# Kernel tuning notes

Measured on AMD Instinct MI355X. Metric: run time of the kernel, lower is better.

The kernel has to match this reference:

```python
import jax, jax.numpy as jnp
import numpy as np

INPUT_DIM = 512
OUTPUT_DIM = 32
DEGREE = 8


def setup_inputs() -> dict:
    key = jax.random.key(0)
    kx, kw = jax.random.split(key)
    x = jax.random.normal(kx, (65536, INPUT_DIM), dtype=jnp.float32)
    # xavier_normal_ on [input_dim, output_dim, degree+1]: torch treats last dims as fan;
    # fan_in = output_dim*(degree+1), fan_out = input_dim*(degree+1)
    fan_in = OUTPUT_DIM * (DEGREE + 1)
    fan_out = INPUT_DIM * (DEGREE + 1)
    std = float(np.sqrt(2.0 / (fan_in + fan_out)))
    cheby_coeffs = std * jax.random.normal(kw, (INPUT_DIM, OUTPUT_DIM, DEGREE + 1), dtype=jnp.float32)
    return {"x": x, "cheby_coeffs": cheby_coeffs}


def reference(x, cheby_coeffs):
    xt = jnp.tanh(x.reshape(-1, INPUT_DIM))
    T = [jnp.ones_like(xt), 2.0 * xt]
    for n in range(2, DEGREE + 1):
        T.append(2.0 * xt * T[n - 1] - T[n - 2])
    T = jnp.stack(T, axis=-1)  # [B, I, degree+1]
    y = jnp.einsum('bij,ioj->bo', T, cheby_coeffs)  # [B, O]
    return y
```

## Files before the change

### kernel.cpp

```cpp
#include <hip/hip_runtime.h>
#include <hip/hip_fp16.h>


typedef _Float16 half8 __attribute__((ext_vector_type(8)));
typedef __fp16  fp16x2 __attribute__((ext_vector_type(2)));
typedef float float4v __attribute__((ext_vector_type(4)));

#define N_I 512
#define N_O 32
#define N_PERIODS 8
#define STEPS 8
#define CHUNK_F16 8192
#define PERIOD_F16 16384
#define PERIOD_BYTES 32768

__global__ void prep(const float* __restrict__ coeffs, _Float16* __restrict__ bsw,
                     float* __restrict__ bias) {
    if (blockIdx.x == 512) {
        int o = threadIdx.x >> 3, p = threadIdx.x & 7;
        float s = 0.f;
        for (int i = p; i < N_I; i += 8) s += coeffs[(i * 32 + o) * 9];
        for (int off = 4; off; off >>= 1) s += __shfl_down(s, off, 8);
        if (p == 0) bias[o] = s;
        return;
    }
    int id = blockIdx.x * 256 + threadIdx.x;
    int jj = id & 7;
    int L  = (id >> 3) & 63;
    int t  = (id >> 9) & 1;
    int s  = id >> 10;
    int ci = s >> 3, sl = s & 7;
    int j  = sl + 1;
    int ii = ((L >> 4) << 3) + jj;
    int i  = ci * 32 + ii;
    int o  = t * 16 + (L & 15);
    bsw[id] = (_Float16)coeffs[(i * 32 + o) * 9 + j];
}

__device__ __forceinline__ float fast_tanh(float v) {
    float e = __expf(2.0f * v);
    return __builtin_fmaf(-2.0f, __builtin_amdgcn_rcpf(e + 1.0f), 1.0f);
}

__device__ __forceinline__ half8 pack8(const float* u) {
    union { fp16x2 h[4]; half8 v; } r;
    r.h[0] = __builtin_amdgcn_cvt_pkrtz(u[0], u[1]);
    r.h[1] = __builtin_amdgcn_cvt_pkrtz(u[2], u[3]);
    r.h[2] = __builtin_amdgcn_cvt_pkrtz(u[4], u[5]);
    r.h[3] = __builtin_amdgcn_cvt_pkrtz(u[6], u[7]);
    return r.v;
}

__global__ __launch_bounds__(256, 2) void cheby_main(
        const float* __restrict__ x, const _Float16* __restrict__ bsw,
        const float* __restrict__ bias, float* __restrict__ y) {
    __shared__ __align__(16) _Float16 bl[2][PERIOD_F16];

    const int tid = threadIdx.x;
    const int wv  = tid >> 6;
    const int L   = tid & 63;
    const int q   = L >> 4;
    const int mr  = L & 15;
    const int m0  = blockIdx.x * 128 + wv * 32;
    const float* xr0 = x + (size_t)(m0 + mr) * N_I + q * 8;
    const float* xr1 = xr0 + 16 * N_I;
    const char* gB = (const char*)bsw;

    float4v acc[2][2];
#pragma unroll
    for (int a = 0; a < 2; ++a)
#pragma unroll
        for (int b = 0; b < 2; ++b)
#pragma unroll
            for (int e = 0; e < 4; ++e) acc[a][b][e] = 0.f;

    auto stage = [&](int p, int buf) {
        const char* gsrc = gB + (size_t)p * PERIOD_BYTES + wv * 8192 + L * 16;
        char* lds = (char*)&bl[buf][0] + wv * 8192;
#pragma unroll
        for (int it = 0; it < 8; ++it) {
            __builtin_amdgcn_global_load_lds(
                (const __attribute__((address_space(1))) void*)(gsrc + it * 1024),
                (__attribute__((address_space(3))) void*)(lds + it * 1024),
                16, 0, 0);
        }
    };

    auto loadx = [&](int p, float4v* v) {
#pragma unroll
        for (int c = 0; c < 2; ++c) {
            const int o = (p * 2 + c) * 32;
            v[c * 4 + 0] = *(const float4v*)(xr0 + o);
            v[c * 4 + 1] = *(const float4v*)(xr0 + o + 4);
            v[c * 4 + 2] = *(const float4v*)(xr1 + o);
            v[c * 4 + 3] = *(const float4v*)(xr1 + o + 4);
        }
    };

    auto chunk = [&](const _Float16* bb, float4v xa, float4v xb,
                     float4v xc, float4v xd) {
        float w0[8], w1[8], up0[8], uc0[8], up1[8], uc1[8];
#pragma unroll
        for (int e = 0; e < 4; ++e) {
            w0[e]     = 2.0f * fast_tanh(xa[e]);
            w0[e + 4] = 2.0f * fast_tanh(xb[e]);
            w1[e]     = 2.0f * fast_tanh(xc[e]);
            w1[e + 4] = 2.0f * fast_tanh(xd[e]);
        }
#pragma unroll
        for (int e = 0; e < 8; ++e) {
            up0[e] = 1.0f; uc0[e] = w0[e];
            up1[e] = 1.0f; uc1[e] = w1[e];
        }
#pragma unroll
        for (int s = 0; s < STEPS; ++s) {
            const half8 a0 = pack8(uc0);
            const half8 a1 = pack8(uc1);
            const half8 b0 = *(const half8*)(bb + (s * 2 + 0) * 512 + L * 8);
            const half8 b1 = *(const half8*)(bb + (s * 2 + 1) * 512 + L * 8);
            acc[0][0] = __builtin_amdgcn_mfma_f32_16x16x32_f16(a0, b0, acc[0][0], 0, 0, 0);
            acc[0][1] = __builtin_amdgcn_mfma_f32_16x16x32_f16(a0, b1, acc[0][1], 0, 0, 0);
            acc[1][0] = __builtin_amdgcn_mfma_f32_16x16x32_f16(a1, b0, acc[1][0], 0, 0, 0);
            acc[1][1] = __builtin_amdgcn_mfma_f32_16x16x32_f16(a1, b1, acc[1][1], 0, 0, 0);
#pragma unroll
            for (int e = 0; e < 8; ++e) {
                float n0 = __builtin_fmaf(w0[e], uc0[e], -up0[e]);
                float n1 = __builtin_fmaf(w1[e], uc1[e], -up1[e]);
                up0[e] = uc0[e]; uc0[e] = n0;
                up1[e] = uc1[e]; uc1[e] = n1;
            }
        }
    };

    float4v cur[8], nxt[8];
    stage(0, 0);
    loadx(0, cur);
    __syncthreads();

    for (int p = 0; p < N_PERIODS; ++p) {
        const int buf = p & 1;
        if (p < N_PERIODS - 1) {
            stage(p + 1, buf ^ 1);
            loadx(p + 1, nxt);
        }
        chunk(&bl[buf][0],    cur[0], cur[1], cur[2], cur[3]);
        chunk(&bl[buf][8192], cur[4], cur[5], cur[6], cur[7]);
#pragma unroll
        for (int k = 0; k < 8; ++k) cur[k] = nxt[k];
        __syncthreads();
    }

    const float b_n0 = bias[mr];
    const float b_n1 = bias[16 + mr];
#pragma unroll
    for (int mt = 0; mt < 2; ++mt) {
#pragma unroll
        for (int e = 0; e < 4; ++e) {
            const int r = m0 + mt * 16 + q * 4 + e;
            y[(size_t)r * N_O + mr]      = acc[mt][0][e] + b_n0;
            y[(size_t)r * N_O + 16 + mr] = acc[mt][1][e] + b_n1;
        }
    }
}

extern "C" void kernel_launch(void* const* d_in, const int* in_sizes, int n_in,
                              void* d_out, int out_size, void* d_ws, size_t ws_size,
                              hipStream_t stream) {
    const float* x      = (const float*)d_in[0];
    const float* coeffs = (const float*)d_in[1];
    float* yout = (float*)d_out;

    _Float16* bsw = (_Float16*)d_ws;
    float* bias   = (float*)((char*)d_ws + 131072 * sizeof(_Float16));

    prep<<<513, 256, 0, stream>>>(coeffs, bsw, bias);
    cheby_main<<<512, 256, 0, stream>>>(x, bsw, bias, yout);
}
```

Before: 215.5 us.

## Run Chebyshev recurrence in packed fp16 and pipeline per chunk with smaller LDS

Moves the Chebyshev recurrence from fp32 FMAs to packed half2 arithmetic, which removes the per-step fp32-to-fp16 packing before each MFMA and halves the recurrence ALU work. The staging granularity drops from 2-chunk periods to single chunks, halving the LDS footprint, and x loads are prefetched two chunks ahead. The factor 2 is folded into the tanh formula. Carrying the recurrence in fp16 risks more accumulated rounding error at higher degrees, and per-chunk barriers double the synchronization count.

Measured after the change: 214.4 us. No clear change (-0.5%).

```diff
diff --git a/kernel.cpp b/kernel.cpp
--- a/kernel.cpp
+++ b/kernel.cpp
@@ -2,17 +2,17 @@
 #include <hip/hip_fp16.h>
 
 
-typedef _Float16 half8 __attribute__((ext_vector_type(8)));
-typedef __fp16  fp16x2 __attribute__((ext_vector_type(2)));
-typedef float float4v __attribute__((ext_vector_type(4)));
+typedef _Float16 half8  __attribute__((ext_vector_type(8)));
+typedef _Float16 half2v __attribute__((ext_vector_type(2)));
+typedef __fp16   fp16x2 __attribute__((ext_vector_type(2)));
+typedef float    float4v __attribute__((ext_vector_type(4)));
 
 #define N_I 512
 #define N_O 32
-#define N_PERIODS 8
+#define N_CHUNKS 16
 #define STEPS 8
 #define CHUNK_F16 8192
-#define PERIOD_F16 16384
-#define PERIOD_BYTES 32768
+#define CHUNK_BYTES 16384
 
 __global__ void prep(const float* __restrict__ coeffs, _Float16* __restrict__ bsw,
                      float* __restrict__ bias) {
@@ -37,24 +37,23 @@
     bsw[id] = (_Float16)coeffs[(i * 32 + o) * 9 + j];
 }
 
-__device__ __forceinline__ float fast_tanh(float v) {
+__device__ __forceinline__ float wfun(float v) {
     float e = __expf(2.0f * v);
-    return __builtin_fmaf(-2.0f, __builtin_amdgcn_rcpf(e + 1.0f), 1.0f);
+    return __builtin_fmaf(-4.0f, __builtin_amdgcn_rcpf(e + 1.0f), 2.0f);
 }
 
-__device__ __forceinline__ half8 pack8(const float* u) {
-    union { fp16x2 h[4]; half8 v; } r;
-    r.h[0] = __builtin_amdgcn_cvt_pkrtz(u[0], u[1]);
-    r.h[1] = __builtin_amdgcn_cvt_pkrtz(u[2], u[3]);
-    r.h[2] = __builtin_amdgcn_cvt_pkrtz(u[4], u[5]);
-    r.h[3] = __builtin_amdgcn_cvt_pkrtz(u[6], u[7]);
-    return r.v;
+__device__ __forceinline__ half2v pkh(float a, float b) {
+    union { fp16x2 f; half2v h; } u;
+    u.f = __builtin_amdgcn_cvt_pkrtz(a, b);
+    return u.h;
 }
+
+union H8 { half2v h2[4]; half8 v; };
 
 __global__ __launch_bounds__(256, 2) void cheby_main(
         const float* __restrict__ x, const _Float16* __restrict__ bsw,
         const float* __restrict__ bias, float* __restrict__ y) {
-    __shared__ __align__(16) _Float16 bl[2][PERIOD_F16];
+    __shared__ __align__(16) _Float16 bl[2][CHUNK_F16];
 
     const int tid = threadIdx.x;
     const int wv  = tid >> 6;
@@ -74,79 +73,81 @@
 #pragma unroll
             for (int e = 0; e < 4; ++e) acc[a][b][e] = 0.f;
 
-    auto stage = [&](int p, int buf) {
-        const char* gsrc = gB + (size_t)p * PERIOD_BYTES + wv * 8192 + L * 16;
-        char* lds = (char*)&bl[buf][0] + wv * 8192;
+    auto stage = [&](int ci, int buf) {
+        const char* gsrc = gB + (size_t)ci * CHUNK_BYTES + wv * 1024 + L * 16;
+        char* lds = (char*)&bl[buf][0] + wv * 1024;
 #pragma unroll
-        for (int it = 0; it < 8; ++it) {
+        for (int it = 0; it < 4; ++it) {
             __builtin_amdgcn_global_load_lds(
-                (const __attribute__((address_space(1))) void*)(gsrc + it * 1024),
-                (__attribute__((address_space(3))) void*)(lds + it * 1024),
+                (const __attribute__((address_space(1))) void*)(gsrc + it * 4096),
+                (__attribute__((address_space(3))) void*)(lds + it * 4096),
                 16, 0, 0);
         }
     };
 
-    auto loadx = [&](int p, float4v* v) {
-#pragma unroll
-        for (int c = 0; c < 2; ++c) {
-            const int o = (p * 2 + c) * 32;
-            v[c * 4 + 0] = *(const float4v*)(xr0 + o);
-            v[c * 4 + 1] = *(const float4v*)(xr0 + o + 4);
-            v[c * 4 + 2] = *(const float4v*)(xr1 + o);
-            v[c * 4 + 3] = *(const float4v*)(xr1 + o + 4);
-        }
+    auto loadx = [&](int ci, float4v* v) {
+        const int o = ci * 32;
+        v[0] = *(const float4v*)(xr0 + o);
+        v[1] = *(const float4v*)(xr0 + o + 4);
+        v[2] = *(const float4v*)(xr1 + o);
+        v[3] = *(const float4v*)(xr1 + o + 4);
     };
 
-    auto chunk = [&](const _Float16* bb, float4v xa, float4v xb,
-                     float4v xc, float4v xd) {
-        float w0[8], w1[8], up0[8], uc0[8], up1[8], uc1[8];
+    const half2v one = {(_Float16)1.0f, (_Float16)1.0f};
+
+    auto chunk = [&](const _Float16* bb, const float4v* xv) {
+        float wf0[8], wf1[8];
 #pragma unroll
         for (int e = 0; e < 4; ++e) {
-            w0[e]     = 2.0f * fast_tanh(xa[e]);
-            w0[e + 4] = 2.0f * fast_tanh(xb[e]);
-            w1[e]     = 2.0f * fast_tanh(xc[e]);
-            w1[e + 4] = 2.0f * fast_tanh(xd[e]);
+            wf0[e]     = wfun(xv[0][e]);
+            wf0[e + 4] = wfun(xv[1][e]);
+            wf1[e]     = wfun(xv[2][e]);
+            wf1[e + 4] = wfun(xv[3][e]);
         }
+        half2v w0[4], w1[4], uc0[4], uc1[4], up0[4], up1[4];
 #pragma unroll
-        for (int e = 0; e < 8; ++e) {
-            up0[e] = 1.0f; uc0[e] = w0[e];
-            up1[e] = 1.0f; uc1[e] = w1[e];
+        for (int h = 0; h < 4; ++h) {
+            w0[h] = pkh(wf0[2 * h], wf0[2 * h + 1]);
+            w1[h] = pkh(wf1[2 * h], wf1[2 * h + 1]);
+            uc0[h] = w0[h]; uc1[h] = w1[h];
+            up0[h] = one;   up1[h] = one;
         }
 #pragma unroll
         for (int s = 0; s < STEPS; ++s) {
-            const half8 a0 = pack8(uc0);
-            const half8 a1 = pack8(uc1);
+            H8 a0, a1;
+#pragma unroll
+            for (int h = 0; h < 4; ++h) { a0.h2[h] = uc0[h]; a1.h2[h] = uc1[h]; }
             const half8 b0 = *(const half8*)(bb + (s * 2 + 0) * 512 + L * 8);
             const half8 b1 = *(const half8*)(bb + (s * 2 + 1) * 512 + L * 8);
-            acc[0][0] = __builtin_amdgcn_mfma_f32_16x16x32_f16(a0, b0, acc[0][0], 0, 0, 0);
-            acc[0][1] = __builtin_amdgcn_mfma_f32_16x16x32_f16(a0, b1, acc[0][1], 0, 0, 0);
-            acc[1][0] = __builtin_amdgcn_mfma_f32_16x16x32_f16(a1, b0, acc[1][0], 0, 0, 0);
-            acc[1][1] = __builtin_amdgcn_mfma_f32_16x16x32_f16(a1, b1, acc[1][1], 0, 0, 0);
+            acc[0][0] = __builtin_amdgcn_mfma_f32_16x16x32_f16(a0.v, b0, acc[0][0], 0, 0, 0);
+            acc[0][1] = __builtin_amdgcn_mfma_f32_16x16x32_f16(a0.v, b1, acc[0][1], 0, 0, 0);
+            acc[1][0] = __builtin_amdgcn_mfma_f32_16x16x32_f16(a1.v, b0, acc[1][0], 0, 0, 0);
+            acc[1][1] = __builtin_amdgcn_mfma_f32_16x16x32_f16(a1.v, b1, acc[1][1], 0, 0, 0);
 #pragma unroll
-            for (int e = 0; e < 8; ++e) {
-                float n0 = __builtin_fmaf(w0[e], uc0[e], -up0[e]);
-                float n1 = __builtin_fmaf(w1[e], uc1[e], -up1[e]);
-                up0[e] = uc0[e]; uc0[e] = n0;
-                up1[e] = uc1[e]; uc1[e] = n1;
+            for (int h = 0; h < 4; ++h) {
+                half2v n0 = w0[h] * uc0[h] - up0[h];
+                half2v n1 = w1[h] * uc1[h] - up1[h];
+                up0[h] = uc0[h]; uc0[h] = n0;
+                up1[h] = uc1[h]; uc1[h] = n1;
             }
         }
     };
 
-    float4v cur[8], nxt[8];
+    float4v xv[2][4];
+    loadx(0, xv[0]);
+    loadx(1, xv[1]);
     stage(0, 0);
-    loadx(0, cur);
     __syncthreads();
 
-    for (int p = 0; p < N_PERIODS; ++p) {
-        const int buf = p & 1;
-        if (p < N_PERIODS - 1) {
-            stage(p + 1, buf ^ 1);
-            loadx(p + 1, nxt);
-        }
-        chunk(&bl[buf][0],    cur[0], cur[1], cur[2], cur[3]);
-        chunk(&bl[buf][8192], cur[4], cur[5], cur[6], cur[7]);
+#pragma unroll 2
+    for (int ci = 0; ci < N_CHUNKS; ++ci) {
+        const int buf = ci & 1;
+        if (ci + 1 < N_CHUNKS) stage(ci + 1, buf ^ 1);
+        float4v xcur[4];
 #pragma unroll
-        for (int k = 0; k < 8; ++k) cur[k] = nxt[k];
+        for (int k = 0; k < 4; ++k) xcur[k] = xv[buf][k];
+        if (ci + 2 < N_CHUNKS) loadx(ci + 2, xv[buf]);
+        chunk(&bl[buf][0], xcur);
         __syncthreads();
     }
 
```
